# Kernel tuning notes

Measured on AMD Instinct MI355X. Metric: run time of the kernel, lower is better.

The kernel has to match this reference:

```python
import jax, jax.numpy as jnp
import numpy as np

# Static problem dims (match input_specs / init_kwargs)
B, NQ, C, H = 2, 900, 256, 8
HGT, WID = 64, 64            # single-scale feature map (input_spatial_shapes = [[64, 64]])
N = HGT * WID                # 4096 keys
DH = C // H                  # head dim 32
RPE_HID = 512
STRIDE = 16                  # feature_stride


def setup_inputs() -> dict:
    key = jax.random.key(0)
    ks = jax.random.split(key, 24)
    p = lambda k, shape: jax.random.normal(k, shape, jnp.float32) * 0.02
    # reference boxes (cx, cy, w, h) in pixel coords of a 1024x1024 image
    ref = jax.random.uniform(ks[0], (B, NQ, 1, 4), jnp.float32)
    ref = jnp.concatenate([ref[..., :2] * (WID * STRIDE), ref[..., 2:] * 128.0], axis=-1)
    return {
        "vggt_features": jnp.zeros((1,), jnp.float32),  # unused by forward (kept for signature fidelity)
        "query": jax.random.normal(ks[1], (B, NQ, C), jnp.float32),
        "reference_2d": ref,
        "k_input_flatten": jax.random.normal(ks[2], (B, N, C), jnp.float32),
        "v_input_flatten": jax.random.normal(ks[3], (B, N, C), jnp.float32),
        "input_spatial_shapes": jnp.array([[HGT, WID]], jnp.int32),
        "input_padding_mask": jnp.zeros((B, N), jnp.bool_),
        # cpb_mlp1 (x) and cpb_mlp2 (y): Linear(2,512)+ReLU+Linear(512,H,no bias); stored as [in,out]
        "W1x": p(ks[4], (2, RPE_HID)), "b1x": jnp.zeros((RPE_HID,), jnp.float32), "W2x": p(ks[5], (RPE_HID, H)),
        "W1y": p(ks[6], (2, RPE_HID)), "b1y": jnp.zeros((RPE_HID,), jnp.float32), "W2y": p(ks[7], (RPE_HID, H)),
        "Wq": p(ks[8], (C, C)), "bq": jnp.zeros((C,), jnp.float32),
        "Wk": p(ks[9], (C, C)), "bk": jnp.zeros((C,), jnp.float32),
        "Wv": p(ks[10], (C, C)), "bv": jnp.zeros((C,), jnp.float32),
        "Wp": p(ks[11], (C, C)), "bp": jnp.zeros((C,), jnp.float32),
    }


def _mlp(d, W1, b1, W2):
    return jax.nn.relu(d @ W1 + b1) @ W2


def reference(vggt_features, query, reference_2d, k_input_flatten, v_input_flatten,
              input_spatial_shapes, input_padding_mask,
              W1x, b1x, W2x, W1y, b1y, W2y, Wq, bq, Wk, bk, Wv, bv, Wp, bp):
    h, w = HGT, WID  # static (input_spatial_shapes[0] == [HGT, WID])
    scale = DH ** -0.5
    # cxcywh -> xyxy: [B, NQ, 1, 4]
    xyxy = jnp.concatenate([reference_2d[..., :2] - reference_2d[..., 2:] / 2,
                            reference_2d[..., :2] + reference_2d[..., 2:] / 2], axis=-1)
    # pixel-center grid coords (linspace(0.5, w-0.5, w) * stride)
    pos_x = ((jnp.arange(w, dtype=jnp.float32) + 0.5) * STRIDE)[None, None, :, None]
    pos_y = ((jnp.arange(h, dtype=jnp.float32) + 0.5) * STRIDE)[None, None, :, None]
    delta_x = xyxy[..., 0::2] - pos_x  # [B, NQ, w, 2]  (x1, x2 rel. to columns)
    delta_y = xyxy[..., 1::2] - pos_y  # [B, NQ, h, 2]  (y1, y2 rel. to rows)
    rpe_x = _mlp(delta_x, W1x, b1x, W2x)  # [B, NQ, w, H]
    rpe_y = _mlp(delta_y, W1y, b1y, W2y)  # [B, NQ, h, H]
    # broadcast add over (row, col) then flatten spatial -> [B, H, NQ, N]
    rpe = (rpe_x[:, :, None] + rpe_y[:, :, :, None]).reshape(B, NQ, h * w, H).transpose(0, 3, 1, 2)
    q = (query @ Wq + bq).reshape(B, NQ, H, DH).transpose(0, 2, 1, 3) * scale  # [B,H,NQ,DH]
    k = (k_input_flatten @ Wk + bk).reshape(B, N, H, DH).transpose(0, 2, 1, 3)  # [B,H,N,DH]
    v = (v_input_flatten @ Wv + bv).reshape(B, N, H, DH).transpose(0, 2, 1, 3)  # [B,H,N,DH]
    attn = jnp.einsum('bhqd,bhkd->bhqk', q, k) + rpe
    attn = attn + input_padding_mask[:, None, None, :].astype(attn.dtype) * (-100.0)
    # torch.clip_ to finfo(min,max) is an identity on finite values; softmax follows
    attn = jax.nn.softmax(attn, axis=-1)
    x = jnp.einsum('bhqk,bhkd->bhqd', attn, v).transpose(0, 2, 1, 3).reshape(B, NQ, C)
    return x @ Wp + bp
```

## Files before the change

### kernel.cpp

```cpp
#include <hip/hip_runtime.h>
#include <hip/hip_bf16.h>
#include <cmath>

#define B_ 2
#define NQ_ 900
#define N_ 4096
#define LOG2E 1.4426950408889634f

typedef __attribute__((ext_vector_type(4))) float f32x4;
typedef __attribute__((ext_vector_type(8))) short s16x8;
typedef __attribute__((ext_vector_type(8))) _Float16 f16x8;

__device__ inline short f2bf(float x) {
    union { __hip_bfloat16 b; short s; } u;
    u.b = __float2bfloat16(x);
    return u.s;
}
__device__ inline short f2h(float x) {
    _Float16 h = (_Float16)x;
    return __builtin_bit_cast(short, h);
}

template <int CTRL>
__device__ inline float dppf(float x) {
    int xi = __builtin_bit_cast(int, x);
    int r = __builtin_amdgcn_update_dpp(xi, xi, CTRL, 0xF, 0xF, true);
    return __builtin_bit_cast(float, r);
}
__device__ inline float rowmax16(float v) {
    v = fmaxf(v, dppf<0x121>(v));
    v = fmaxf(v, dppf<0x122>(v));
    v = fmaxf(v, dppf<0x124>(v));
    v = fmaxf(v, dppf<0x128>(v));
    return v;
}
__device__ inline float rowsum16(float v) {
    v += dppf<0x121>(v);
    v += dppf<0x122>(v);
    v += dppf<0x124>(v);
    v += dppf<0x128>(v);
    return v;
}

__global__ __launch_bounds__(256) void proj_kernel(
    const float* __restrict__ query, const float* __restrict__ kin,
    const float* __restrict__ vin,
    const float* __restrict__ Wq, const float* __restrict__ Wk,
    const float* __restrict__ Wv,
    const float* __restrict__ bqv, const float* __restrict__ bkv,
    const float* __restrict__ bvv,
    unsigned short* __restrict__ qbf, unsigned short* __restrict__ kbf,
    unsigned short* __restrict__ vbf, float qscale)
{
    const int mtx = blockIdx.z;
    const float* X = mtx == 0 ? query : mtx == 1 ? kin : vin;
    const float* W = mtx == 0 ? Wq : mtx == 1 ? Wk : Wv;
    const float* bias = mtx == 0 ? bqv : mtx == 1 ? bkv : bvv;
    unsigned short* Y = mtx == 0 ? qbf : mtx == 1 ? kbf : vbf;
    const int M = mtx == 0 ? 1800 : 8192;
    const int m0 = blockIdx.x * 64;
    if (m0 >= M) return;
    const float alpha = mtx == 0 ? qscale : 1.0f;
    const int rows_per_b = mtx == 0 ? 900 : 4096;
    const int ROWS = mtx == 0 ? 960 : 4096;

    __shared__ short Ab[16384];
    __shared__ short Bb[16384];
    const int tid = threadIdx.x;
    const int w = tid >> 6, l = tid & 63, quad = l >> 4, l15 = l & 15;
    const int wq = tid & 3, mm = tid >> 2;

    {
        const bool valid = (m0 + mm) < M;
        const float* xr = X + (size_t)(m0 + mm) * 256;
        #pragma unroll
        for (int it = 0; it < 8; ++it) {
            int g2 = it * 4 + wq;
            float4 a0 = make_float4(0.f, 0.f, 0.f, 0.f), a1 = a0;
            if (valid) {
                a0 = *(const float4*)(xr + g2 * 8);
                a1 = *(const float4*)(xr + g2 * 8 + 4);
            }
            uint4 pk;
            pk.x = (unsigned)(unsigned short)f2bf(a0.x) | ((unsigned)(unsigned short)f2bf(a0.y) << 16);
            pk.y = (unsigned)(unsigned short)f2bf(a0.z) | ((unsigned)(unsigned short)f2bf(a0.w) << 16);
            pk.z = (unsigned)(unsigned short)f2bf(a1.x) | ((unsigned)(unsigned short)f2bf(a1.y) << 16);
            pk.w = (unsigned)(unsigned short)f2bf(a1.z) | ((unsigned)(unsigned short)f2bf(a1.w) << 16);
            *(uint4*)(Ab + (it * 256 + mm * 4 + wq) * 8) = pk;
        }
    }

    for (int nt0 = 0; nt0 < 4; ++nt0) {
        const int n0 = nt0 * 64;
        {
            const float* wcol = W + n0 + mm;
            #pragma unroll
            for (int it = 0; it < 8; ++it) {
                int g2 = it * 4 + wq;
                uint4 wk4;
                wk4.x = (unsigned)(unsigned short)f2bf(wcol[(g2 * 8 + 0) * 256])
                      | ((unsigned)(unsigned short)f2bf(wcol[(g2 * 8 + 1) * 256]) << 16);
                wk4.y = (unsigned)(unsigned short)f2bf(wcol[(g2 * 8 + 2) * 256])
                      | ((unsigned)(unsigned short)f2bf(wcol[(g2 * 8 + 3) * 256]) << 16);
                wk4.z = (unsigned)(unsigned short)f2bf(wcol[(g2 * 8 + 4) * 256])
                      | ((unsigned)(unsigned short)f2bf(wcol[(g2 * 8 + 5) * 256]) << 16);
                wk4.w = (unsigned)(unsigned short)f2bf(wcol[(g2 * 8 + 6) * 256])
                      | ((unsigned)(unsigned short)f2bf(wcol[(g2 * 8 + 7) * 256]) << 16);
                *(uint4*)(Bb + (it * 256 + mm * 4 + wq) * 8) = wk4;
            }
        }
        __syncthreads();

        f32x4 acc[4] = {{0.f,0.f,0.f,0.f},{0.f,0.f,0.f,0.f},{0.f,0.f,0.f,0.f},{0.f,0.f,0.f,0.f}};
        #pragma unroll
        for (int kc = 0; kc < 8; ++kc) {
            s16x8 a = *(const s16x8*)(Ab + (kc * 256 + (w * 16 + l15) * 4 + quad) * 8);
            #pragma unroll
            for (int nt = 0; nt < 4; ++nt) {
                s16x8 bf = *(const s16x8*)(Bb + (kc * 256 + (nt * 16 + l15) * 4 + quad) * 8);
                acc[nt] = __builtin_amdgcn_mfma_f32_16x16x32_bf16(a, bf, acc[nt], 0, 0, 0);
            }
        }
        __syncthreads();

        #pragma unroll
        for (int nt = 0; nt < 4; ++nt) {
            int n = n0 + nt * 16 + l15;
            float bs = bias[n];
            int h = n >> 5, d = n & 31;
            #pragma unroll
            for (int r = 0; r < 4; ++r) {
                int row = m0 + w * 16 + quad * 4 + r;
                if (row < M) {
                    int b = row / rows_per_b;
                    int pos = row - b * rows_per_b;
                    Y[((size_t)(b * 8 + h) * ROWS + pos) * 32 + d] =
                        (unsigned short)f2bf((acc[nt][r] + bs) * alpha);
                }
            }
        }
    }
}

__global__ __launch_bounds__(256) void outproj_kernel(
    const float* __restrict__ X, const float* __restrict__ W,
    const float* __restrict__ bias, float* __restrict__ Y, int M)
{
    __shared__ short Abh[4096], Abl[4096], Bbh[4096], Bbl[4096];
    const int tid = threadIdx.x;
    const int m0 = blockIdx.x * 64, n0 = blockIdx.y * 64;
    const int w = tid >> 6, l = tid & 63, quad = l >> 4, l15 = l & 15;
    const int wq = tid & 3, mm = tid >> 2;
    const bool valid = (m0 + mm) < M;
    const float* xr = X + (size_t)(m0 + mm) * 256;
    const float* wcol = W + n0 + mm;

    f32x4 acc[4] = {{0.f,0.f,0.f,0.f},{0.f,0.f,0.f,0.f},{0.f,0.f,0.f,0.f},{0.f,0.f,0.f,0.f}};

    for (int kq = 0; kq < 4; ++kq) {
        #pragma unroll
        for (int it = 0; it < 2; ++it) {
            int g2 = it * 4 + wq;
            int kbase = kq * 64 + g2 * 8;
            float av[8], bv[8];
            #pragma unroll
            for (int j = 0; j < 8; ++j) {
                av[j] = valid ? xr[kbase + j] : 0.f;
                bv[j] = wcol[(kbase + j) * 256];
            }
            uint4 ah, al, bh, bl;
            unsigned* ahp = (unsigned*)&ah; unsigned* alp = (unsigned*)&al;
            unsigned* bhp = (unsigned*)&bh; unsigned* blp = (unsigned*)&bl;
            #pragma unroll
            for (int j2 = 0; j2 < 4; ++j2) {
                _Float16 h0 = (_Float16)av[j2 * 2], h1 = (_Float16)av[j2 * 2 + 1];
                ahp[j2] = (unsigned)(unsigned short)__builtin_bit_cast(short, h0)
                        | ((unsigned)(unsigned short)__builtin_bit_cast(short, h1) << 16);
                alp[j2] = (unsigned)(unsigned short)f2h(av[j2 * 2] - (float)h0)
                        | ((unsigned)(unsigned short)f2h(av[j2 * 2 + 1] - (float)h1) << 16);
                _Float16 g0 = (_Float16)bv[j2 * 2], g1 = (_Float16)bv[j2 * 2 + 1];
                bhp[j2] = (unsigned)(unsigned short)__builtin_bit_cast(short, g0)
                        | ((unsigned)(unsigned short)__builtin_bit_cast(short, g1) << 16);
                blp[j2] = (unsigned)(unsigned short)f2h(bv[j2 * 2] - (float)g0)
                        | ((unsigned)(unsigned short)f2h(bv[j2 * 2 + 1] - (float)g1) << 16);
            }
            int gi = (it * 256 + mm * 4 + wq) * 8;
            *(uint4*)(Abh + gi) = ah;
            *(uint4*)(Abl + gi) = al;
            *(uint4*)(Bbh + gi) = bh;
            *(uint4*)(Bbl + gi) = bl;
        }
        __syncthreads();

        #pragma unroll
        for (int kc = 0; kc < 2; ++kc) {
            int ga = (kc * 256 + (w * 16 + l15) * 4 + quad) * 8;
            f16x8 ah = *(const f16x8*)(Abh + ga);
            f16x8 al = *(const f16x8*)(Abl + ga);
            #pragma unroll
            for (int nt = 0; nt < 4; ++nt) {
                int gb = (kc * 256 + (nt * 16 + l15) * 4 + quad) * 8;
                f16x8 bh = *(const f16x8*)(Bbh + gb);
                f16x8 bl = *(const f16x8*)(Bbl + gb);
                acc[nt] = __builtin_amdgcn_mfma_f32_16x16x32_f16(ah, bh, acc[nt], 0, 0, 0);
                acc[nt] = __builtin_amdgcn_mfma_f32_16x16x32_f16(ah, bl, acc[nt], 0, 0, 0);
                acc[nt] = __builtin_amdgcn_mfma_f32_16x16x32_f16(al, bh, acc[nt], 0, 0, 0);
            }
        }
        __syncthreads();
    }

    #pragma unroll
    for (int nt = 0; nt < 4; ++nt) {
        int n = n0 + nt * 16 + l15;
        float bs = bias[n];
        #pragma unroll
        for (int r = 0; r < 4; ++r) {
            int row = m0 + w * 16 + quad * 4 + r;
            if (row < M)
                Y[(size_t)row * 256 + n] = acc[nt][r] + bs;
        }
    }
}

__global__ __launch_bounds__(512) void rpe3_kernel(
    const float* __restrict__ ref2d,
    const float* __restrict__ W1x, const float* __restrict__ b1x,
    const float* __restrict__ W1y, const float* __restrict__ b1y,
    const float* __restrict__ W2x, const float* __restrict__ W2y,
    float* __restrict__ rpe_x, float* __restrict__ rpe_y)
{
    __shared__ short sw2h[8192], sw2l[8192];
    __shared__ float4 sW1p[576];
    __shared__ float2 sB1p[576];

    const int tid = threadIdx.x;
    for (int i = tid; i < 8192; i += 512) {
        int g = i >> 3, j = i & 7;
        int kcg = g >> 6, rr = g & 63, n = rr >> 2, q4 = rr & 3;
        int k = kcg * 32 + q4 * 8 + j;
        float val = ((n < 8) ? W2x[k * 8 + n] : W2y[k * 8 + (n - 8)]) * LOG2E;
        _Float16 hi = (_Float16)val;
        sw2h[i] = __builtin_bit_cast(short, hi);
        sw2l[i] = f2h(val - (float)hi);
    }
    if (tid < 512) {
        int i = tid;
        sW1p[(i >> 3) * 9 + (i & 7)] = make_float4(W1x[i], W1x[512 + i], W1y[i], W1y[512 + i]);
        sB1p[(i >> 3) * 9 + (i & 7)] = make_float2(b1x[i], b1y[i]);
    }

    const int w = tid >> 6, l = tid & 63, quad = l >> 4, l15 = l & 15;
    const int qi = w >> 2, wrow = w & 3;
    const int bq = blockIdx.x * 2 + qi;
    const float4 box = *(const float4*)(ref2d + (size_t)bq * 4);
    const int row = wrow * 16 + l15;
    const float pc = (row + 0.5f) * 16.0f;
    const float dx0 = (box.x - box.z * 0.5f) - pc;
    const float dx1 = (box.x + box.z * 0.5f) - pc;
    const float dy0 = (box.y - box.w * 0.5f) - pc;
    const float dy1 = (box.y + box.w * 0.5f) - pc;

    __syncthreads();

    f32x4 accx = {0.f, 0.f, 0.f, 0.f}, accy = {0.f, 0.f, 0.f, 0.f};
    for (int kc = 0; kc < 16; ++kc) {
        f16x8 axh, axl, ayh, ayl;
        #pragma unroll
        for (int i = 0; i < 8; ++i) {
            int gi = (kc * 4 + quad) * 9 + i;
            float4 w1 = sW1p[gi];
            float2 bb = sB1p[gi];
            float hx = fmaxf(fmaf(dx0, w1.x, fmaf(dx1, w1.y, bb.x)), 0.f);
            float hy = fmaxf(fmaf(dy0, w1.z, fmaf(dy1, w1.w, bb.y)), 0.f);
            _Float16 xh = (_Float16)hx;
            _Float16 yh = (_Float16)hy;
            axh[i] = xh;
            axl[i] = (_Float16)(hx - (float)xh);
            ayh[i] = yh;
            ayl[i] = (_Float16)(hy - (float)yh);
        }
        f16x8 bh = *(const f16x8*)(sw2h + (kc * 64 + l15 * 4 + quad) * 8);
        f16x8 bl = *(const f16x8*)(sw2l + (kc * 64 + l15 * 4 + quad) * 8);
        accx = __builtin_amdgcn_mfma_f32_16x16x32_f16(axh, bh, accx, 0, 0, 0);
        accx = __builtin_amdgcn_mfma_f32_16x16x32_f16(axh, bl, accx, 0, 0, 0);
        accx = __builtin_amdgcn_mfma_f32_16x16x32_f16(axl, bh, accx, 0, 0, 0);
        accy = __builtin_amdgcn_mfma_f32_16x16x32_f16(ayh, bh, accy, 0, 0, 0);
        accy = __builtin_amdgcn_mfma_f32_16x16x32_f16(ayh, bl, accy, 0, 0, 0);
        accy = __builtin_amdgcn_mfma_f32_16x16x32_f16(ayl, bh, accy, 0, 0, 0);
    }

    #pragma unroll
    for (int rr = 0; rr < 4; ++rr) {
        int row_out = wrow * 16 + quad * 4 + rr;
        size_t base = ((size_t)bq * 64 + row_out) * 8;
        if (l15 < 8) rpe_x[base + l15] = accx[rr];
        else         rpe_y[base + (l15 - 8)] = accy[rr];
    }
}

__global__ __launch_bounds__(512, 4) void attn_mfma_kernel(
    const unsigned short* __restrict__ qb16, const unsigned short* __restrict__ kb16,
    const unsigned short* __restrict__ vb16,
    const float* __restrict__ rpe_x, const float* __restrict__ rpe_y,
    const unsigned char* __restrict__ mask, float* __restrict__ xout)
{
    __shared__ short skf[4 * 2048];
    __shared__ short svt[4 * 2048];
    __shared__ short spb[8 * 544];
    __shared__ float ry[32 * 65];
    __shared__ unsigned long long smaskb[64];
    __shared__ float sm[8][16], sl[8][16], sLf[32];

    const int tid = threadIdx.x;
    const int qb = blockIdx.x, h = blockIdx.y, b = blockIdx.z;
    const int q0 = qb * 32;
    const int w = tid >> 6, l = tid & 63;
    const int qsub = w >> 2, g = w & 3;
    const int quad = l >> 4, l15 = l & 15;

    const unsigned short* qg = qb16 + (size_t)(b * 8 + h) * 960 * 32;
    const unsigned short* kg = kb16 + (size_t)(b * 8 + h) * 4096 * 32;
    const unsigned short* vg = vb16 + (size_t)(b * 8 + h) * 4096 * 32;

    for (int i = tid; i < 2048; i += 512) {
        int qq = q0 + (i >> 6), pos = i & 63;
        float vy = 0.f;
        if (qq < NQ_)
            vy = rpe_y[((size_t)(b * NQ_ + qq) * 64 + pos) * 8 + h];
        ry[(i >> 6) * 65 + pos] = vy;
    }
    #pragma unroll
    for (int j = 0; j < 8; ++j) {
        int c = w * 8 + j;
        unsigned long long bits = __ballot(mask[(size_t)b * N_ + c * 64 + l] != 0);
        if (l == 0) smaskb[c] = bits;
    }

    s16x8 qa = *(const s16x8*)(qg + (size_t)(q0 + qsub * 16 + l15) * 32 + quad * 8);

    f32x4 rx4[4];
    #pragma unroll
    for (int t = 0; t < 4; ++t)
        #pragma unroll
        for (int r = 0; r < 4; ++r) {
            int qq = q0 + qsub * 16 + quad * 4 + r;
            rx4[t][r] = (qq < NQ_)
                ? rpe_x[((size_t)(b * NQ_ + qq) * 64 + t * 16 + l15) * 8 + h] : 0.f;
        }

    const int sg = tid >> 7, role = (tid >> 6) & 1, stl = tid & 63;
    int eoff[4];
    if (role == 0) {
        #pragma unroll
        for (int t = 0; t < 4; ++t)
            eoff[t] = (t * 16 + (stl & 15)) * 32 + (stl >> 4) * 8;
    } else {
        #pragma unroll
        for (int t = 0; t < 4; ++t)
            eoff[t] = stl * 32 + t * 8;
    }
    const unsigned short* src = role ? vg : kg;

    uint4 pf[4];
    {
        size_t cb = (size_t)(sg * 16) * 2048;
        #pragma unroll
        for (int t = 0; t < 4; ++t) pf[t] = *(const uint4*)(src + cb + eoff[t]);
    }

    float mrow[4] = {-INFINITY, -INFINITY, -INFINITY, -INFINITY};
    float lrow[4] = {0.f, 0.f, 0.f, 0.f};
    f32x4 acc0 = {0.f, 0.f, 0.f, 0.f}, acc1 = {0.f, 0.f, 0.f, 0.f};
    short* pw = spb + w * 544;

    for (int i = 0; i < 16; ++i) {
        __syncthreads();
        if (role == 0) {
            #pragma unroll
            for (int t = 0; t < 4; ++t)
                *(uint4*)(skf + sg * 2048 + (t * 64 + stl) * 8) = pf[t];
        } else {
            short* vtw = svt + sg * 2048;
            #pragma unroll
            for (int t = 0; t < 4; ++t) {
                const unsigned short* pv = (const unsigned short*)&pf[t];
                #pragma unroll
                for (int j = 0; j < 8; ++j) {
                    int d = t * 8 + j;
                    vtw[d * 64 + (((stl >> 3) ^ (d & 7)) << 3) + (stl & 7)] = (short)pv[j];
                }
            }
        }
        __syncthreads();

        {
            int inext = (i + 1 < 16) ? i + 1 : 15;
            size_t cb = (size_t)(sg * 16 + inext) * 2048;
            #pragma unroll
            for (int t = 0; t < 4; ++t) pf[t] = *(const uint4*)(src + cb + eoff[t]);
        }

        const int cgc = g * 16 + i;
        const short* kf = skf + g * 2048;

        f32x4 sc[4];
        #pragma unroll
        for (int t = 0; t < 4; ++t) {
            s16x8 kb = *(const s16x8*)(kf + (t * 64 + l) * 8);
            sc[t] = __builtin_amdgcn_mfma_f32_16x16x32_bf16(qa, kb, rx4[t], 0, 0, 0);
        }
        float ryv[4];
        #pragma unroll
        for (int r = 0; r < 4; ++r)
            ryv[r] = ry[(qsub * 16 + quad * 4 + r) * 65 + cgc];
        unsigned long long mb = smaskb[cgc];
        if (mb) {
            #pragma unroll
            for (int t = 0; t < 4; ++t) {
                float mk = ((mb >> (t * 16 + l15)) & 1ULL) ? -144.2695f : 0.f;
                #pragma unroll
                for (int r = 0; r < 4; ++r) sc[t][r] += mk;
            }
        }
        #pragma unroll
        for (int t = 0; t < 4; ++t)
            #pragma unroll
            for (int r = 0; r < 4; ++r)
                sc[t][r] += ryv[r];

        float cm[4];
        #pragma unroll
        for (int r = 0; r < 4; ++r) {
            cm[r] = fmaxf(fmaxf(sc[0][r], sc[1][r]), fmaxf(sc[2][r], sc[3][r]));
            cm[r] = rowmax16(cm[r]);
        }
        float al[4];
        #pragma unroll
        for (int r = 0; r < 4; ++r) {
            float mnew = fmaxf(mrow[r], cm[r]);
            al[r] = exp2f(mrow[r] - mnew);
            mrow[r] = mnew;
            lrow[r] *= al[r];
            acc0[r] *= al[r];
            acc1[r] *= al[r];
        }
        #pragma unroll
        for (int t = 0; t < 4; ++t)
            #pragma unroll
            for (int r = 0; r < 4; ++r)
                sc[t][r] = exp2f(sc[t][r] - mrow[r]);
        #pragma unroll
        for (int r = 0; r < 4; ++r) {
            float rs = (sc[0][r] + sc[1][r]) + (sc[2][r] + sc[3][r]);
            lrow[r] += rowsum16(rs);
        }

        const short* vt = svt + g * 2048;
        #pragma unroll
        for (int hh = 0; hh < 2; ++hh) {
            #pragma unroll
            for (int tt = 0; tt < 2; ++tt) {
                int t = hh * 2 + tt;
                int gphys = (tt * 2 + (l15 >> 3)) ^ quad;
                #pragma unroll
                for (int r = 0; r < 4; ++r)
                    pw[(gphys * 17 + quad * 4 + r) * 8 + (l15 & 7)] = f2bf(sc[t][r]);
            }
            int gph_r = quad ^ (l15 >> 2);
            s16x8 pa  = *(const s16x8*)(pw + (gph_r * 17 + l15) * 8);
            int ksw = ((hh * 4 + quad) ^ (l15 & 7)) * 8;
            s16x8 vb0 = *(const s16x8*)(vt + l15 * 64 + ksw);
            s16x8 vb1 = *(const s16x8*)(vt + (16 + l15) * 64 + ksw);
            acc0 = __builtin_amdgcn_mfma_f32_16x16x32_bf16(pa, vb0, acc0, 0, 0, 0);
            acc1 = __builtin_amdgcn_mfma_f32_16x16x32_bf16(pa, vb1, acc1, 0, 0, 0);
        }
    }

    __syncthreads();
    if (l15 == 0) {
        #pragma unroll
        for (int r = 0; r < 4; ++r) {
            sm[w][quad * 4 + r] = mrow[r];
            sl[w][quad * 4 + r] = lrow[r];
        }
    }
    __syncthreads();
    float wgt[4], L4[4];
    #pragma unroll
    for (int r = 0; r < 4; ++r) {
        int qrow = quad * 4 + r;
        float mm = -INFINITY;
        #pragma unroll
        for (int gg = 0; gg < 4; ++gg) mm = fmaxf(mm, sm[qsub * 4 + gg][qrow]);
        float LL = 0.f;
        #pragma unroll
        for (int gg = 0; gg < 4; ++gg)
            LL += exp2f(sm[qsub * 4 + gg][qrow] - mm) * sl[qsub * 4 + gg][qrow];
        wgt[r] = exp2f(mrow[r] - mm);
        L4[r] = LL;
    }
    if (g == 0 && l15 == 0) {
        #pragma unroll
        for (int r = 0; r < 4; ++r) sLf[qsub * 16 + quad * 4 + r] = L4[r];
    }

    float* obuf = (float*)skf;
    for (int gg = 0; gg < 4; ++gg) {
        if (g == gg) {
            #pragma unroll
            for (int r = 0; r < 4; ++r) {
                int idx = (qsub * 16 + quad * 4 + r) * 33 + l15;
                float v0 = wgt[r] * acc0[r];
                float v1 = wgt[r] * acc1[r];
                if (gg == 0) { obuf[idx] = v0; obuf[idx + 16] = v1; }
                else         { obuf[idx] += v0; obuf[idx + 16] += v1; }
            }
        }
        __syncthreads();
    }

    for (int i = tid; i < 1024; i += 512) {
        int ql = i >> 5, d = i & 31;
        int qq = q0 + ql;
        if (qq < NQ_)
            xout[(size_t)(b * NQ_ + qq) * 256 + h * 32 + d] = obuf[ql * 33 + d] / sLf[ql];
    }
}

extern "C" void kernel_launch(void* const* d_in, const int* in_sizes, int n_in,
                              void* d_out, int out_size, void* d_ws, size_t ws_size,
                              hipStream_t stream)
{
    const float* query = (const float*)d_in[1];
    const float* ref2d = (const float*)d_in[2];
    const float* kin   = (const float*)d_in[3];
    const float* vin   = (const float*)d_in[4];
    const unsigned char* mask = (const unsigned char*)d_in[6];
    const float* W1x = (const float*)d_in[7];
    const float* b1x = (const float*)d_in[8];
    const float* W2x = (const float*)d_in[9];
    const float* W1y = (const float*)d_in[10];
    const float* b1y = (const float*)d_in[11];
    const float* W2y = (const float*)d_in[12];
    const float* Wq  = (const float*)d_in[13];
    const float* bq  = (const float*)d_in[14];
    const float* Wk  = (const float*)d_in[15];
    const float* bk  = (const float*)d_in[16];
    const float* Wv  = (const float*)d_in[17];
    const float* bv  = (const float*)d_in[18];
    const float* Wp  = (const float*)d_in[19];
    const float* bp  = (const float*)d_in[20];

    char* wsb = (char*)d_ws;
    unsigned short* qbf = (unsigned short*)(wsb);
    unsigned short* kbf = (unsigned short*)(wsb +   983040);
    unsigned short* vbf = (unsigned short*)(wsb +  5177344);
    float* rxws = (float*)(wsb +  9371648);
    float* ryws = (float*)(wsb + 13058048);
    float* xws  = (float*)(wsb + 16744448);
    float* out  = (float*)d_out;

    const float qscale = LOG2E / sqrtf(32.0f);

    proj_kernel<<<dim3(128, 1, 3), 256, 0, stream>>>(
        query, kin, vin, Wq, Wk, Wv, bq, bk, bv, qbf, kbf, vbf, qscale);
    rpe3_kernel<<<900, 512, 0, stream>>>(
        ref2d, W1x, b1x, W1y, b1y, W2x, W2y, rxws, ryws);
    attn_mfma_kernel<<<dim3(29, 8, B_), 512, 0, stream>>>(
        qbf, kbf, vbf, rxws, ryws, mask, xws);
    outproj_kernel<<<dim3(29, 4), 256, 0, stream>>>(xws, Wp, bp, out, 1800);
}
```

Baseline: 245.7 us.

## Pre-transpose V in projection and load K/V fragments directly from global

The projection kernel now writes V in a per-chunk transposed (d-major) layout by staging through shared memory. The attention kernel drops its shared-memory K/V staging, prefetch and barriers, and each wave loads its MFMA K and V fragments straight from global (L2) memory. The attention block shrinks to 16 queries and 256 threads, doubling the grid. This removes LDS traffic and per-chunk syncs. In exchange, K/V reuse across the query sub-tiles of a block is lost, so each K/V chunk is re-read from cache by twice as many blocks.

```diff
diff --git a/kernel.cpp b/kernel.cpp
--- a/kernel.cpp
+++ b/kernel.cpp
@@ -50,13 +50,12 @@
     const float* __restrict__ bqv, const float* __restrict__ bkv,
     const float* __restrict__ bvv,
     unsigned short* __restrict__ qbf, unsigned short* __restrict__ kbf,
-    unsigned short* __restrict__ vbf, float qscale)
+    unsigned short* __restrict__ vtb, float qscale)
 {
     const int mtx = blockIdx.z;
     const float* X = mtx == 0 ? query : mtx == 1 ? kin : vin;
     const float* W = mtx == 0 ? Wq : mtx == 1 ? Wk : Wv;
     const float* bias = mtx == 0 ? bqv : mtx == 1 ? bkv : bvv;
-    unsigned short* Y = mtx == 0 ? qbf : mtx == 1 ? kbf : vbf;
     const int M = mtx == 0 ? 1800 : 8192;
     const int m0 = blockIdx.x * 64;
     if (m0 >= M) return;
@@ -123,21 +122,44 @@
         }
         __syncthreads();
 
-        #pragma unroll
-        for (int nt = 0; nt < 4; ++nt) {
-            int n = n0 + nt * 16 + l15;
-            float bs = bias[n];
-            int h = n >> 5, d = n & 31;
-            #pragma unroll
-            for (int r = 0; r < 4; ++r) {
-                int row = m0 + w * 16 + quad * 4 + r;
-                if (row < M) {
-                    int b = row / rows_per_b;
-                    int pos = row - b * rows_per_b;
-                    Y[((size_t)(b * 8 + h) * ROWS + pos) * 32 + d] =
-                        (unsigned short)f2bf((acc[nt][r] + bs) * alpha);
+        if (mtx < 2) {
+            unsigned short* Y = mtx == 0 ? qbf : kbf;
+            #pragma unroll
+            for (int nt = 0; nt < 4; ++nt) {
+                int n = n0 + nt * 16 + l15;
+                float bs = bias[n];
+                int h = n >> 5, d = n & 31;
+                #pragma unroll
+                for (int r = 0; r < 4; ++r) {
+                    int row = m0 + w * 16 + quad * 4 + r;
+                    if (row < M) {
+                        int b = row / rows_per_b;
+                        int pos = row - b * rows_per_b;
+                        Y[((size_t)(b * 8 + h) * ROWS + pos) * 32 + d] =
+                            (unsigned short)f2bf((acc[nt][r] + bs) * alpha);
+                    }
                 }
             }
+        } else {
+            #pragma unroll
+            for (int nt = 0; nt < 4; ++nt) {
+                float bs = bias[n0 + nt * 16 + l15];
+                #pragma unroll
+                for (int r = 0; r < 4; ++r)
+                    Bb[(nt * 16 + l15) * 72 + (w * 16 + quad * 4 + r)] =
+                        f2bf(acc[nt][r] + bs);
+            }
+            __syncthreads();
+            const int b = m0 >> 12, c = (m0 >> 6) & 63;
+            #pragma unroll
+            for (int p = 0; p < 2; ++p) {
+                int j = p * 256 + tid;
+                int nl = j >> 3, k0 = (j & 7) * 8;
+                int n = n0 + nl, h = n >> 5, d = n & 31;
+                *(uint4*)(vtb + (((size_t)(b * 8 + h) * 64 + c) * 2048 + d * 64 + k0)) =
+                    *(const uint4*)(Bb + nl * 72 + k0);
+            }
+            __syncthreads();
         }
     }
 }
@@ -299,31 +321,29 @@
     }
 }
 
-__global__ __launch_bounds__(512, 4) void attn_mfma_kernel(
+__global__ __launch_bounds__(256, 4) void attn_mfma_kernel(
     const unsigned short* __restrict__ qb16, const unsigned short* __restrict__ kb16,
-    const unsigned short* __restrict__ vb16,
+    const unsigned short* __restrict__ vtb,
     const float* __restrict__ rpe_x, const float* __restrict__ rpe_y,
     const unsigned char* __restrict__ mask, float* __restrict__ xout)
 {
-    __shared__ short skf[4 * 2048];
-    __shared__ short svt[4 * 2048];
-    __shared__ short spb[8 * 544];
-    __shared__ float ry[32 * 65];
+    __shared__ short spb[4 * 544];
+    __shared__ float ry[16 * 65];
     __shared__ unsigned long long smaskb[64];
-    __shared__ float sm[8][16], sl[8][16], sLf[32];
+    __shared__ float sm[4][16], sl[4][16], sLf[16];
 
     const int tid = threadIdx.x;
     const int qb = blockIdx.x, h = blockIdx.y, b = blockIdx.z;
-    const int q0 = qb * 32;
+    const int q0 = qb * 16;
     const int w = tid >> 6, l = tid & 63;
-    const int qsub = w >> 2, g = w & 3;
+    const int g = w;
     const int quad = l >> 4, l15 = l & 15;
 
     const unsigned short* qg = qb16 + (size_t)(b * 8 + h) * 960 * 32;
     const unsigned short* kg = kb16 + (size_t)(b * 8 + h) * 4096 * 32;
-    const unsigned short* vg = vb16 + (size_t)(b * 8 + h) * 4096 * 32;
-
-    for (int i = tid; i < 2048; i += 512) {
+    const unsigned short* vtg = vtb + (size_t)(b * 8 + h) * 64 * 2048;
+
+    for (int i = tid; i < 1024; i += 256) {
         int qq = q0 + (i >> 6), pos = i & 63;
         float vy = 0.f;
         if (qq < NQ_)
@@ -331,90 +351,55 @@
         ry[(i >> 6) * 65 + pos] = vy;
     }
     #pragma unroll
-    for (int j = 0; j < 8; ++j) {
-        int c = w * 8 + j;
+    for (int j = 0; j < 16; ++j) {
+        int c = w * 16 + j;
         unsigned long long bits = __ballot(mask[(size_t)b * N_ + c * 64 + l] != 0);
         if (l == 0) smaskb[c] = bits;
     }
 
-    s16x8 qa = *(const s16x8*)(qg + (size_t)(q0 + qsub * 16 + l15) * 32 + quad * 8);
+    s16x8 qa = *(const s16x8*)(qg + (size_t)(q0 + l15) * 32 + quad * 8);
 
     f32x4 rx4[4];
     #pragma unroll
     for (int t = 0; t < 4; ++t)
         #pragma unroll
         for (int r = 0; r < 4; ++r) {
-            int qq = q0 + qsub * 16 + quad * 4 + r;
+            int qq = q0 + quad * 4 + r;
             rx4[t][r] = (qq < NQ_)
                 ? rpe_x[((size_t)(b * NQ_ + qq) * 64 + t * 16 + l15) * 8 + h] : 0.f;
         }
 
-    const int sg = tid >> 7, role = (tid >> 6) & 1, stl = tid & 63;
-    int eoff[4];
-    if (role == 0) {
-        #pragma unroll
-        for (int t = 0; t < 4; ++t)
-            eoff[t] = (t * 16 + (stl & 15)) * 32 + (stl >> 4) * 8;
-    } else {
-        #pragma unroll
-        for (int t = 0; t < 4; ++t)
-            eoff[t] = stl * 32 + t * 8;
-    }
-    const unsigned short* src = role ? vg : kg;
-
-    uint4 pf[4];
-    {
-        size_t cb = (size_t)(sg * 16) * 2048;
-        #pragma unroll
-        for (int t = 0; t < 4; ++t) pf[t] = *(const uint4*)(src + cb + eoff[t]);
-    }
-
+    __syncthreads();
     float mrow[4] = {-INFINITY, -INFINITY, -INFINITY, -INFINITY};
     float lrow[4] = {0.f, 0.f, 0.f, 0.f};
     f32x4 acc0 = {0.f, 0.f, 0.f, 0.f}, acc1 = {0.f, 0.f, 0.f, 0.f};
     short* pw = spb + w * 544;
 
     for (int i = 0; i < 16; ++i) {
-        __syncthreads();
-        if (role == 0) {
-            #pragma unroll
-            for (int t = 0; t < 4; ++t)
-                *(uint4*)(skf + sg * 2048 + (t * 64 + stl) * 8) = pf[t];
-        } else {
-            short* vtw = svt + sg * 2048;
-            #pragma unroll
-            for (int t = 0; t < 4; ++t) {
-                const unsigned short* pv = (const unsigned short*)&pf[t];
-                #pragma unroll
-                for (int j = 0; j < 8; ++j) {
-                    int d = t * 8 + j;
-                    vtw[d * 64 + (((stl >> 3) ^ (d & 7)) << 3) + (stl & 7)] = (short)pv[j];
-                }
-            }
-        }
-        __syncthreads();
-
-        {
-            int inext = (i + 1 < 16) ? i + 1 : 15;
-            size_t cb = (size_t)(sg * 16 + inext) * 2048;
-            #pragma unroll
-            for (int t = 0; t < 4; ++t) pf[t] = *(const uint4*)(src + cb + eoff[t]);
-        }
-
-        const int cgc = g * 16 + i;
-        const short* kf = skf + g * 2048;
+        const int c = g * 16 + i;
+
+        uint4 kf[4];
+        #pragma unroll
+        for (int t = 0; t < 4; ++t)
+            kf[t] = *(const uint4*)(kg + ((size_t)c * 64 + t * 16 + l15) * 32 + quad * 8);
+        uint4 vf[4];
+        #pragma unroll
+        for (int hh = 0; hh < 2; ++hh) {
+            vf[hh * 2]     = *(const uint4*)(vtg + (size_t)c * 2048 + l15 * 64        + hh * 32 + quad * 8);
+            vf[hh * 2 + 1] = *(const uint4*)(vtg + (size_t)c * 2048 + (16 + l15) * 64 + hh * 32 + quad * 8);
+        }
 
         f32x4 sc[4];
         #pragma unroll
         for (int t = 0; t < 4; ++t) {
-            s16x8 kb = *(const s16x8*)(kf + (t * 64 + l) * 8);
+            s16x8 kb = __builtin_bit_cast(s16x8, kf[t]);
             sc[t] = __builtin_amdgcn_mfma_f32_16x16x32_bf16(qa, kb, rx4[t], 0, 0, 0);
         }
         float ryv[4];
         #pragma unroll
         for (int r = 0; r < 4; ++r)
-            ryv[r] = ry[(qsub * 16 + quad * 4 + r) * 65 + cgc];
-        unsigned long long mb = smaskb[cgc];
+            ryv[r] = ry[(quad * 4 + r) * 65 + c];
+        unsigned long long mb = smaskb[c];
         if (mb) {
             #pragma unroll
             for (int t = 0; t < 4; ++t) {
@@ -456,7 +441,6 @@
             lrow[r] += rowsum16(rs);
         }
 
-        const short* vt = svt + g * 2048;
         #pragma unroll
         for (int hh = 0; hh < 2; ++hh) {
             #pragma unroll
@@ -468,10 +452,9 @@
                     pw[(gphys * 17 + quad * 4 + r) * 8 + (l15 & 7)] = f2bf(sc[t][r]);
             }
             int gph_r = quad ^ (l15 >> 2);
-            s16x8 pa  = *(const s16x8*)(pw + (gph_r * 17 + l15) * 8);
-            int ksw = ((hh * 4 + quad) ^ (l15 & 7)) * 8;
-            s16x8 vb0 = *(const s16x8*)(vt + l15 * 64 + ksw);
-            s16x8 vb1 = *(const s16x8*)(vt + (16 + l15) * 64 + ksw);
+            s16x8 pa = *(const s16x8*)(pw + (gph_r * 17 + l15) * 8);
+            s16x8 vb0 = __builtin_bit_cast(s16x8, vf[hh * 2]);
+            s16x8 vb1 = __builtin_bit_cast(s16x8, vf[hh * 2 + 1]);
             acc0 = __builtin_amdgcn_mfma_f32_16x16x32_bf16(pa, vb0, acc0, 0, 0, 0);
             acc1 = __builtin_amdgcn_mfma_f32_16x16x32_bf16(pa, vb1, acc1, 0, 0, 0);
         }
@@ -492,25 +475,25 @@
         int qrow = quad * 4 + r;
         float mm = -INFINITY;
         #pragma unroll
-        for (int gg = 0; gg < 4; ++gg) mm = fmaxf(mm, sm[qsub * 4 + gg][qrow]);
+        for (int gg = 0; gg < 4; ++gg) mm = fmaxf(mm, sm[gg][qrow]);
         float LL = 0.f;
         #pragma unroll
         for (int gg = 0; gg < 4; ++gg)
-            LL += exp2f(sm[qsub * 4 + gg][qrow] - mm) * sl[qsub * 4 + gg][qrow];
+            LL += exp2f(sm[gg][qrow] - mm) * sl[gg][qrow];
         wgt[r] = exp2f(mrow[r] - mm);
         L4[r] = LL;
     }
     if (g == 0 && l15 == 0) {
         #pragma unroll
-        for (int r = 0; r < 4; ++r) sLf[qsub * 16 + quad * 4 + r] = L4[r];
-    }
-
-    float* obuf = (float*)skf;
+        for (int r = 0; r < 4; ++r) sLf[quad * 4 + r] = L4[r];
+    }
+
+    float* obuf = (float*)spb;
     for (int gg = 0; gg < 4; ++gg) {
         if (g == gg) {
             #pragma unroll
             for (int r = 0; r < 4; ++r) {
-                int idx = (qsub * 16 + quad * 4 + r) * 33 + l15;
+                int idx = (quad * 4 + r) * 33 + l15;
                 float v0 = wgt[r] * acc0[r];
                 float v1 = wgt[r] * acc1[r];
                 if (gg == 0) { obuf[idx] = v0; obuf[idx + 16] = v1; }
@@ -520,7 +503,7 @@
         __syncthreads();
     }
 
-    for (int i = tid; i < 1024; i += 512) {
+    for (int i = tid; i < 512; i += 256) {
         int ql = i >> 5, d = i & 31;
         int qq = q0 + ql;
         if (qq < NQ_)
@@ -555,7 +538,7 @@
     char* wsb = (char*)d_ws;
     unsigned short* qbf = (unsigned short*)(wsb);
     unsigned short* kbf = (unsigned short*)(wsb +   983040);
-    unsigned short* vbf = (unsigned short*)(wsb +  5177344);
+    unsigned short* vtb = (unsigned short*)(wsb +  5177344);
     float* rxws = (float*)(wsb +  9371648);
     float* ryws = (float*)(wsb + 13058048);
     float* xws  = (float*)(wsb + 16744448);
@@ -564,10 +547,10 @@
     const float qscale = LOG2E / sqrtf(32.0f);
 
     proj_kernel<<<dim3(128, 1, 3), 256, 0, stream>>>(
-        query, kin, vin, Wq, Wk, Wv, bq, bk, bv, qbf, kbf, vbf, qscale);
+        query, kin, vin, Wq, Wk, Wv, bq, bk, bv, qbf, kbf, vtb, qscale);
     rpe3_kernel<<<900, 512, 0, stream>>>(
         ref2d, W1x, b1x, W1y, b1y, W2x, W2y, rxws, ryws);
-    attn_mfma_kernel<<<dim3(29, 8, B_), 512, 0, stream>>>(
-        qbf, kbf, vbf, rxws, ryws, mask, xws);
+    attn_mfma_kernel<<<dim3(57, 8, B_), 256, 0, stream>>>(
+        qbf, kbf, vtb, rxws, ryws, mask, xws);
     outproj_kernel<<<dim3(29, 4), 256, 0, stream>>>(xws, Wp, bp, out, 1800);
 }
```

After: 246.9 us. No clear change (+0.5%).
